# Performance work log

Measured on AMD Instinct MI355X. Metric: run time of the kernel, lower is better.

Reference implementation:

```python
import math
import jax, jax.numpy as jnp
import numpy as np

B, L, D, H = 4, 4096, 1024, 16
DK = D // H


def setup_inputs() -> dict:
    key = jax.random.key(0)
    ks = jax.random.split(key, 11)
    s = 0.02
    return {
        "queries": jax.random.normal(ks[0], (B, L, D), jnp.float32),
        "keys": jax.random.normal(ks[1], (B, L, D), jnp.float32),
        "values": jax.random.normal(ks[2], (B, L, D), jnp.float32),
        "Wq": jax.random.normal(ks[3], (D, D), jnp.float32) * s,
        "bq": jnp.zeros((D,), jnp.float32),
        "Wk": jax.random.normal(ks[4], (D, D), jnp.float32) * s,
        "bk": jnp.zeros((D,), jnp.float32),
        "Wv": jax.random.normal(ks[5], (D, D), jnp.float32) * s,
        "bv": jnp.zeros((D,), jnp.float32),
        "Wo": jax.random.normal(ks[6], (D, D), jnp.float32) * s,
        "bo": jnp.zeros((D,), jnp.float32),
    }


def reference(queries, keys, values, Wq, bq, Wk, bk, Wv, bv, Wo, bo):
    # projections + split heads: (B, H, L, DK)
    q = (queries @ Wq + bq).reshape(B, L, H, DK).transpose(0, 2, 1, 3)
    k = (keys @ Wk + bk).reshape(B, L, H, DK).transpose(0, 2, 1, 3)
    v = (values @ Wv + bv).reshape(B, L, H, DK).transpose(0, 2, 1, 3)

    # per-head mean over channel dim -> (B, H, L)
    qm = q.mean(axis=-1)
    km = k.mean(axis=-1)

    # FFT-based autocorrelation: corr (B, H, L)
    qf = jnp.fft.rfft(qm, axis=-1)
    kf = jnp.fft.rfft(km, axis=-1)
    corr = jnp.fft.irfft(qf * jnp.conj(kf), n=L, axis=-1)

    top_k = max(1, int(math.log(L)))  # top_k=None path -> 8 for L=4096
    w, delays = jax.lax.top_k(corr, top_k)          # (B, H, K)
    w = jax.nn.softmax(w, axis=-1)

    # torch.roll(x, shift=d): out[i] = x[(i - d) mod L]
    pos = jnp.arange(L)
    out = jnp.zeros_like(v)
    for kk in range(top_k):
        idx = (pos[None, None, :] - delays[:, :, kk, None]) % L  # (B, H, L)
        rolled = jnp.take_along_axis(v, idx[..., None], axis=2)  # (B, H, L, DK)
        out = out + w[:, :, kk, None, None] * rolled

    # merge heads (matches per-head concat order) and output projection
    out = out.transpose(0, 2, 1, 3).reshape(B, L, D)
    return out @ Wo + bo
```

## Files before the change

### kernel.cpp

```cpp
#include <hip/hip_runtime.h>
#include <hip/hip_bf16.h>
#include <cstdint>

#define BB 4
#define LL 4096
#define DD 1024
#define HH 16
#define DKH 64
#define MROWS 16384
#define KTOP 8
#define RPB 16

typedef float f32x4 __attribute__((ext_vector_type(4)));
typedef _Float16 f16;
typedef _Float16 f16x4 __attribute__((ext_vector_type(4)));
typedef _Float16 f16x8 __attribute__((ext_vector_type(8)));

__device__ __forceinline__ void gll16(const void* g, void* l) {
    __builtin_amdgcn_global_load_lds(
        (const __attribute__((address_space(1))) void*)g,
        (__attribute__((address_space(3))) void*)l, 16, 0, 0);
}

template <int CTRL>
__device__ __forceinline__ float dppf(float x) {
    return __builtin_bit_cast(float,
        __builtin_amdgcn_update_dpp(0, __builtin_bit_cast(int, x), CTRL, 0xF, 0xF, true));
}

__global__ void k_colmeans(const float* __restrict__ Wq, const float* __restrict__ bq,
                           const float* __restrict__ Wk, const float* __restrict__ bk,
                           float* __restrict__ Wqm_t, float* __restrict__ Wkm_t,
                           float* __restrict__ bqm, float* __restrict__ bkm) {
    int t = blockIdx.x * blockDim.x + threadIdx.x;
    int which = t >> 14;
    int idx = t & 16383;
    int d = idx >> 4;
    int h = idx & 15;
    const float* W = which ? Wk : Wq;
    const float* p = W + d * DD + h * DKH;
    float s = 0.f;
    #pragma unroll
    for (int c = 0; c < DKH; ++c) s += p[c];
    (which ? Wkm_t : Wqm_t)[h * DD + d] = s * (1.0f / DKH);
    if (d == 0) {
        const float* bb = which ? bk : bq;
        float sb = 0.f;
        for (int c = 0; c < DKH; ++c) sb += bb[h * DKH + c];
        (which ? bkm : bqm)[h] = sb * (1.0f / DKH);
    }
}

__global__ void k_transpose_cvt(const float* __restrict__ in, f16* __restrict__ out) {
    __shared__ float tile[32][33];
    int k0 = blockIdx.x * 32;
    int n0 = blockIdx.y * 32;
    int tx = threadIdx.x, ty = threadIdx.y;
    #pragma unroll
    for (int j = 0; j < 32; j += 8)
        tile[ty + j][tx] = in[(k0 + ty + j) * DD + n0 + tx];
    __syncthreads();
    #pragma unroll
    for (int j = 0; j < 32; j += 8)
        out[(n0 + ty + j) * DD + k0 + tx] = (f16)tile[tx][ty + j];
}

__global__ void k_cvt_f16(const float* __restrict__ in, f16* __restrict__ out) {
    int i = blockIdx.x * blockDim.x + threadIdx.x;
    f32x4 v = ((const f32x4*)in)[i];
    f16x4 o;
    o[0] = (f16)v.x; o[1] = (f16)v.y; o[2] = (f16)v.z; o[3] = (f16)v.w;
    ((f16x4*)out)[i] = o;
}

__global__ __launch_bounds__(256, 4) void k_means(const float* __restrict__ q, const float* __restrict__ k,
                        const float* __restrict__ Wqm_t, const float* __restrict__ Wkm_t,
                        const float* __restrict__ bqm, const float* __restrict__ bkm,
                        float* __restrict__ qm, float* __restrict__ km) {
    __shared__ float lred[RPB * 264];
    int isK = blockIdx.x & 1;
    int rb  = blockIdx.x >> 1;
    const float* src = isK ? k : q;
    const float* W   = isK ? Wkm_t : Wqm_t;
    const float* bm  = isK ? bkm : bqm;
    float* dst = isK ? km : qm;
    int t = threadIdx.x;
    int wavei = t >> 6, lane = t & 63;
    int c = wavei * 256 + lane * 4;
    f32x4 wr[16];
    #pragma unroll
    for (int h = 0; h < 16; ++h) wr[h] = *(const f32x4*)(W + h * DD + c);
    #pragma unroll
    for (int h = 0; h < 16; ++h) asm volatile("" : "+v"(wr[h]));
    const float* rbase = src + (size_t)rb * RPB * DD + c;
    f32x4 rv = *(const f32x4*)rbase;
    #pragma unroll
    for (int r = 0; r < RPB; ++r) {
        f32x4 nxt = rv;
        if (r + 1 < RPB) nxt = *(const f32x4*)(rbase + (r + 1) * DD);
        float v[16];
        #pragma unroll
        for (int h = 0; h < 16; ++h)
            v[h] = rv.x * wr[h].x + rv.y * wr[h].y + rv.z * wr[h].z + rv.w * wr[h].w;
        float u[8];
        #pragma unroll
        for (int i = 0; i < 8; ++i) {
            float keep = (lane & 1) ? v[2*i+1] : v[2*i];
            float send = (lane & 1) ? v[2*i]   : v[2*i+1];
            u[i] = keep + dppf<0xB1>(send);
        }
        float w2[4];
        #pragma unroll
        for (int i = 0; i < 4; ++i) {
            float keep = (lane & 2) ? u[2*i+1] : u[2*i];
            float send = (lane & 2) ? u[2*i]   : u[2*i+1];
            w2[i] = keep + dppf<0x4E>(send);
        }
        float y[2];
        #pragma unroll
        for (int i = 0; i < 2; ++i) {
            float keep = (lane & 8) ? w2[2*i+1] : w2[2*i];
            float send = (lane & 8) ? w2[2*i]   : w2[2*i+1];
            y[i] = keep + dppf<0x128>(send);
        }
        {
            float keep = (lane & 4) ? y[1] : y[0];
            float send = (lane & 4) ? y[0] : y[1];
            float z = keep + __shfl_xor(send, 4);
            lred[r * 264 + wavei * 64 + lane] = z;
        }
        rv = nxt;
    }
    __syncthreads();
    int rr = t >> 4, h = t & 15;
    int lp = (h & 3) | (((h >> 2) & 1) << 3) | (((h >> 3) & 1) << 2);
    float s = bm[h];
    #pragma unroll
    for (int w = 0; w < 4; ++w)
        #pragma unroll
        for (int g = 0; g < 4; ++g)
            s += lred[rr * 264 + w * 64 + g * 16 + lp];
    int row = rb * RPB + rr;
    int b = row >> 12, l = row & 4095;
    dst[((size_t)((b << 4) + h) << 12) + l] = s;
}

__global__ __launch_bounds__(1024) void k_corr(const float* __restrict__ qm,
                                               const float* __restrict__ km,
                                               float* __restrict__ corr) {
    __shared__ float sq[LL];
    __shared__ f32x4 red[1024];
    int bh = blockIdx.x >> 2;
    int lag0 = (blockIdx.x & 3) * 1024;
    const f32x4* qg = (const f32x4*)(qm + bh * LL);
    const f32x4* kg = (const f32x4*)(km + bh * LL);
    f32x4* sq4 = (f32x4*)sq;
    int t = threadIdx.x;
    for (int i = t; i < LL / 4; i += 1024) sq4[i] = qg[i];
    __syncthreads();
    int lt = t & 255;
    int ms = t >> 8;
    int d0 = lag0 + lt * 4;
    int m0 = ms * 1024;
    float a0 = 0, a1 = 0, a2 = 0, a3 = 0;
    f32x4 wv = sq4[((m0 + d0) & 4095) >> 2];
    float w0 = wv.x, w1 = wv.y, w2 = wv.z, w3 = wv.w;
    #pragma unroll 4
    for (int m = m0; m < m0 + 1024; m += 4) {
        f32x4 nx = sq4[((m + 4 + d0) & 4095) >> 2];
        int mi = __builtin_amdgcn_readfirstlane(m >> 2);
        f32x4 kv = kg[mi];
        a0 += kv.x * w0;  a1 += kv.x * w1;  a2 += kv.x * w2;  a3 += kv.x * w3;
        a0 += kv.y * w1;  a1 += kv.y * w2;  a2 += kv.y * w3;  a3 += kv.y * nx.x;
        a0 += kv.z * w2;  a1 += kv.z * w3;  a2 += kv.z * nx.x; a3 += kv.z * nx.y;
        a0 += kv.w * w3;  a1 += kv.w * nx.x; a2 += kv.w * nx.y; a3 += kv.w * nx.z;
        w0 = nx.x; w1 = nx.y; w2 = nx.z; w3 = nx.w;
    }
    f32x4 p; p.x = a0; p.y = a1; p.z = a2; p.w = a3;
    red[t] = p;
    __syncthreads();
    if (t < 256) {
        f32x4 s0 = red[t], s1 = red[256 + t], s2 = red[512 + t], s3 = red[768 + t];
        f32x4 s;
        s.x = s0.x + s1.x + s2.x + s3.x;
        s.y = s0.y + s1.y + s2.y + s3.y;
        s.z = s0.z + s1.z + s2.z + s3.z;
        s.w = s0.w + s1.w + s2.w + s3.w;
        *(f32x4*)(corr + bh * LL + lag0 + t * 4) = s;
    }
}

__global__ __launch_bounds__(256) void k_topk(const float* __restrict__ corr,
                                              float* __restrict__ wts, int* __restrict__ dls) {
    __shared__ float sc[LL];
    __shared__ float rv[4]; __shared__ int ri[4];
    __shared__ float topv[KTOP]; __shared__ int topi[KTOP];
    int bh = blockIdx.x;
    for (int i = threadIdx.x; i < LL; i += 256) sc[i] = corr[bh * LL + i];
    for (int kk = 0; kk < KTOP; ++kk) {
        __syncthreads();
        float bv = -1e30f; int bi = 0;
        for (int i = threadIdx.x; i < LL; i += 256) {
            float v = sc[i];
            if (v > bv) { bv = v; bi = i; }
        }
        #pragma unroll
        for (int off = 32; off; off >>= 1) {
            float ov = __shfl_down(bv, off);
            int oi = __shfl_down(bi, off);
            if (ov > bv || (ov == bv && oi < bi)) { bv = ov; bi = oi; }
        }
        int wid = threadIdx.x >> 6;
        if ((threadIdx.x & 63) == 0) { rv[wid] = bv; ri[wid] = bi; }
        __syncthreads();
        if (threadIdx.x == 0) {
            for (int w = 1; w < 4; ++w)
                if (rv[w] > bv || (rv[w] == bv && ri[w] < bi)) { bv = rv[w]; bi = ri[w]; }
            topv[kk] = bv; topi[kk] = bi;
            sc[bi] = -1e30f;
        }
    }
    __syncthreads();
    if (threadIdx.x == 0) {
        float mx = topv[0], s = 0.f, e[KTOP];
        #pragma unroll
        for (int kk = 0; kk < KTOP; ++kk) { e[kk] = __expf(topv[kk] - mx); s += e[kk]; }
        float inv = 1.0f / s;
        #pragma unroll
        for (int kk = 0; kk < KTOP; ++kk) {
            wts[bh * KTOP + kk] = e[kk] * inv;
            dls[bh * KTOP + kk] = topi[kk];
        }
    }
}

#define BM 128
#define BN 128
#define BKK 32
template <int MODE>
__global__ __launch_bounds__(256) void k_gemm_bt(const f16* __restrict__ A,
                                                 const f16* __restrict__ BT,
                                                 const float* __restrict__ bias,
                                                 void* __restrict__ Cout) {
    __shared__ f16 As[BM * BKK];
    __shared__ f16 Bs[BN * BKK];
    const int K = DD;
    int m0 = blockIdx.x * BM;
    int n0 = blockIdx.y * BN;
    int tid = threadIdx.x;
    int lane = tid & 63;
    int wave = tid >> 6;
    int wm = wave & 1, wn = wave >> 1;

    int row0 = tid >> 2;
    int slot = tid & 3;
    int kc0 = slot ^ ((row0 >> 1) & 3);
    int row1 = row0 + 64;
    int kc1 = slot ^ ((row1 >> 1) & 3);
    const f16* gA0 = A + (size_t)(m0 + row0) * K + kc0 * 8;
    const f16* gA1 = A + (size_t)(m0 + row1) * K + kc1 * 8;
    const f16* gB0 = BT + (size_t)(n0 + row0) * K + kc0 * 8;
    const f16* gB1 = BT + (size_t)(n0 + row1) * K + kc1 * 8;
    char* ldsA0 = (char*)As + wave * 1024;
    char* ldsA1 = (char*)As + 4096 + wave * 1024;
    char* ldsB0 = (char*)Bs + wave * 1024;
    char* ldsB1 = (char*)Bs + 4096 + wave * 1024;

    int fr = lane & 15;
    int quad = lane >> 4;
    int a_off[4], b_off[4];
    #pragma unroll
    for (int i = 0; i < 4; ++i) {
        int ra = wm * 64 + i * 16 + fr;
        a_off[i] = (ra * 4 + (quad ^ ((ra >> 1) & 3))) * 8;
        int rb = wn * 64 + i * 16 + fr;
        b_off[i] = (rb * 4 + (quad ^ ((rb >> 1) & 3))) * 8;
    }

    f32x4 acc[4][4] = {};
    for (int kt = 0; kt < K; kt += BKK) {
        __syncthreads();
        gll16(gA0, ldsA0);
        gll16(gA1, ldsA1);
        gll16(gB0, ldsB0);
        gll16(gB1, ldsB1);
        gA0 += BKK; gA1 += BKK; gB0 += BKK; gB1 += BKK;
        __syncthreads();
        f16x8 af[4], bf[4];
        #pragma unroll
        for (int i = 0; i < 4; ++i) af[i] = *(const f16x8*)(As + a_off[i]);
        #pragma unroll
        for (int i = 0; i < 4; ++i) bf[i] = *(const f16x8*)(Bs + b_off[i]);
        #pragma unroll
        for (int im = 0; im < 4; ++im)
            #pragma unroll
            for (int in = 0; in < 4; ++in)
                acc[im][in] = __builtin_amdgcn_mfma_f32_16x16x32_f16(af[im], bf[in], acc[im][in], 0, 0, 0);
    }

    #pragma unroll
    for (int in = 0; in < 4; ++in) {
        int col = n0 + wn * 64 + in * 16 + fr;
        float bb = bias[col];
        #pragma unroll
        for (int im = 0; im < 4; ++im) {
            int rowb = m0 + wm * 64 + im * 16 + quad * 4;
            #pragma unroll
            for (int r = 0; r < 4; ++r) {
                float val = acc[im][in][r] + bb;
                if (MODE == 0) {
                    int rr = rowb + r;
                    int b = rr >> 12, l = rr & 4095, h = col >> 6, c = col & 63;
                    ((f16*)Cout)[((size_t)(((b << 4) + h) << 12) + l) * 64 + c] = (f16)val;
                } else {
                    ((float*)Cout)[(size_t)(rowb + r) * DD + col] = val;
                }
            }
        }
    }
}

__global__ __launch_bounds__(256) void k_roll(const f16* __restrict__ V,
                                              const float* __restrict__ wts,
                                              const int* __restrict__ dls,
                                              f16* __restrict__ out) {
    int t = blockIdx.x * 256 + threadIdx.x;
    int cc = t & 7;
    int l = (t >> 3) & 4095;
    int bh = t >> 15;
    const f16* vb = V + ((size_t)bh << 18);
    float a[8] = {};
    #pragma unroll
    for (int kk = 0; kk < KTOP; ++kk) {
        float w = wts[bh * KTOP + kk];
        int d = dls[bh * KTOP + kk];
        int src = (l - d) & 4095;
        f16x8 vv = *(const f16x8*)(vb + (src << 6) + (cc << 3));
        #pragma unroll
        for (int j = 0; j < 8; ++j) a[j] += w * (float)vv[j];
    }
    f16* o = out + ((size_t)((bh >> 4) << 12) + l) * 1024 + ((bh & 15) << 6) + (cc << 3);
    f16x8 ov;
    #pragma unroll
    for (int j = 0; j < 8; ++j) ov[j] = (f16)a[j];
    *(f16x8*)o = ov;
}

extern "C" void kernel_launch(void* const* d_in, const int* in_sizes, int n_in,
                              void* d_out, int out_size, void* d_ws, size_t ws_size,
                              hipStream_t stream) {
    const float* queries = (const float*)d_in[0];
    const float* keys    = (const float*)d_in[1];
    const float* values  = (const float*)d_in[2];
    const float* Wq = (const float*)d_in[3];
    const float* bq = (const float*)d_in[4];
    const float* Wk = (const float*)d_in[5];
    const float* bk = (const float*)d_in[6];
    const float* Wv = (const float*)d_in[7];
    const float* bv = (const float*)d_in[8];
    const float* Wo = (const float*)d_in[9];
    const float* bo = (const float*)d_in[10];

    char* ws = (char*)d_ws;
    size_t off = 0;
    auto alloc = [&](size_t bytes) -> char* {
        char* p = ws + off;
        off += (bytes + 255) & ~(size_t)255;
        return p;
    };
    f16*   values_f16 = (f16*)alloc((size_t)MROWS * DD * 2);
    f16*   Vbuf       = (f16*)alloc((size_t)MROWS * DD * 2);
    f16*   WvT        = (f16*)alloc((size_t)DD * DD * 2);
    f16*   WoT        = (f16*)alloc((size_t)DD * DD * 2);
    float* Wqm_t      = (float*)alloc(HH * DD * 4);
    float* Wkm_t      = (float*)alloc(HH * DD * 4);
    float* bqm        = (float*)alloc(HH * 4);
    float* bkm        = (float*)alloc(HH * 4);
    float* qm         = (float*)alloc((size_t)BB * HH * LL * 4);
    float* km         = (float*)alloc((size_t)BB * HH * LL * 4);
    float* corr       = (float*)alloc((size_t)BB * HH * LL * 4);
    float* wts        = (float*)alloc(BB * HH * KTOP * 4);
    int*   dls        = (int*)alloc(BB * HH * KTOP * 4);
    f16*   out_f16    = values_f16;

    k_colmeans<<<128, 256, 0, stream>>>(Wq, bq, Wk, bk, Wqm_t, Wkm_t, bqm, bkm);
    k_transpose_cvt<<<dim3(32, 32), dim3(32, 8), 0, stream>>>(Wv, WvT);
    k_transpose_cvt<<<dim3(32, 32), dim3(32, 8), 0, stream>>>(Wo, WoT);
    k_cvt_f16<<<16384, 256, 0, stream>>>(values, values_f16);
    k_means<<<2048, 256, 0, stream>>>(queries, keys, Wqm_t, Wkm_t, bqm, bkm, qm, km);
    k_corr<<<256, 1024, 0, stream>>>(qm, km, corr);
    k_topk<<<64, 256, 0, stream>>>(corr, wts, dls);
    k_gemm_bt<0><<<dim3(MROWS / BM, DD / BN), 256, 0, stream>>>(values_f16, WvT, bv, Vbuf);
    k_roll<<<8192, 256, 0, stream>>>(Vbuf, wts, dls, out_f16);
    k_gemm_bt<1><<<dim3(MROWS / BM, DD / BN), 256, 0, stream>>>(out_f16, WoT, bo, d_out);
}
```

Measured before the change: 443.8 us.

## Double-buffer GEMM LDS tiles and remap roll kernel block order

The GEMM kernel now uses two LDS buffers, issuing the global-to-LDS load for the next K tile before computing on the current one, so each iteration needs one barrier instead of two and load latency can overlap the MFMA work. LDS use doubles per block, which may lower occupancy. The roll kernel also permutes block indices so that consecutive launched blocks spread across different regions of the work, aiming for better cache or channel locality in the gathered V reads. The single-barrier scheme depends on the asynchronous LDS load being finished by the next barrier.

```diff
diff --git a/kernel.cpp b/kernel.cpp
--- a/kernel.cpp
+++ b/kernel.cpp
@@ -242,8 +242,8 @@
                                                  const f16* __restrict__ BT,
                                                  const float* __restrict__ bias,
                                                  void* __restrict__ Cout) {
-    __shared__ f16 As[BM * BKK];
-    __shared__ f16 Bs[BN * BKK];
+    __shared__ f16 As[2][BM * BKK];
+    __shared__ f16 Bs[2][BN * BKK];
     const int K = DD;
     int m0 = blockIdx.x * BM;
     int n0 = blockIdx.y * BN;
@@ -261,10 +261,6 @@
     const f16* gA1 = A + (size_t)(m0 + row1) * K + kc1 * 8;
     const f16* gB0 = BT + (size_t)(n0 + row0) * K + kc0 * 8;
     const f16* gB1 = BT + (size_t)(n0 + row1) * K + kc1 * 8;
-    char* ldsA0 = (char*)As + wave * 1024;
-    char* ldsA1 = (char*)As + 4096 + wave * 1024;
-    char* ldsB0 = (char*)Bs + wave * 1024;
-    char* ldsB1 = (char*)Bs + 4096 + wave * 1024;
 
     int fr = lane & 15;
     int quad = lane >> 4;
@@ -278,25 +274,40 @@
     }
 
     f32x4 acc[4][4] = {};
-    for (int kt = 0; kt < K; kt += BKK) {
-        __syncthreads();
-        gll16(gA0, ldsA0);
-        gll16(gA1, ldsA1);
-        gll16(gB0, ldsB0);
-        gll16(gB1, ldsB1);
+
+    auto STAGE = [&](int b) {
+        char* la = (char*)As + b * 8192 + wave * 1024;
+        char* lb = (char*)Bs + b * 8192 + wave * 1024;
+        gll16(gA0, la);
+        gll16(gA1, la + 4096);
+        gll16(gB0, lb);
+        gll16(gB1, lb + 4096);
         gA0 += BKK; gA1 += BKK; gB0 += BKK; gB1 += BKK;
-        __syncthreads();
+    };
+    auto COMPUTE = [&](int b) {
+        const f16* Ab = As[b];
+        const f16* Bb = Bs[b];
         f16x8 af[4], bf[4];
         #pragma unroll
-        for (int i = 0; i < 4; ++i) af[i] = *(const f16x8*)(As + a_off[i]);
-        #pragma unroll
-        for (int i = 0; i < 4; ++i) bf[i] = *(const f16x8*)(Bs + b_off[i]);
+        for (int i = 0; i < 4; ++i) af[i] = *(const f16x8*)(Ab + a_off[i]);
+        #pragma unroll
+        for (int i = 0; i < 4; ++i) bf[i] = *(const f16x8*)(Bb + b_off[i]);
         #pragma unroll
         for (int im = 0; im < 4; ++im)
             #pragma unroll
             for (int in = 0; in < 4; ++in)
                 acc[im][in] = __builtin_amdgcn_mfma_f32_16x16x32_f16(af[im], bf[in], acc[im][in], 0, 0, 0);
-    }
+    };
+
+    STAGE(0);
+    __syncthreads();
+    const int NT = K / BKK;
+    for (int kt = 0; kt < NT - 1; ++kt) {
+        STAGE((kt & 1) ^ 1);
+        COMPUTE(kt & 1);
+        __syncthreads();
+    }
+    COMPUTE((NT - 1) & 1);
 
     #pragma unroll
     for (int in = 0; in < 4; ++in) {
@@ -324,7 +335,9 @@
                                               const float* __restrict__ wts,
                                               const int* __restrict__ dls,
                                               f16* __restrict__ out) {
-    int t = blockIdx.x * 256 + threadIdx.x;
+    int x = blockIdx.x;
+    int wk = ((x & 7) << 10) | (x >> 3);
+    int t = wk * 256 + threadIdx.x;
     int cc = t & 7;
     int l = (t >> 3) & 4095;
     int bh = t >> 15;
```

After: 449.0 us. About the same (+1.2%).
